# Kernel tuning notes

Hardware: AMD Instinct MI355X
Metric: run time of the kernel (lower is better)

Reference implementation:

```python
import jax, jax.numpy as jnp
import numpy as np

# dims: T time steps, B batch, CIN/COUT conv channels, HxW spatial, K kernel
T, B, CIN, COUT, H, Wd, K = 10, 32, 3, 64, 64, 64, 3
DECAY = 0.2      # LIF leak factor
INH = 1.625      # lateral inhibition strength (mode='threshold')


def setup_inputs() -> dict:
    key = jax.random.key(0)
    k1, k2 = jax.random.split(key)
    x = (jax.random.uniform(k1, (T, B, CIN, H, Wd)) < 0.2).astype(jnp.float32)
    W = jax.random.normal(k2, (COUT, CIN, K, K), dtype=jnp.float32)
    # normweight(): zero-mean, unit-std (biased) per output filter
    W = W - W.mean(axis=(1, 2, 3), keepdims=True)
    W = W / W.reshape(COUT, -1).std(axis=1).reshape(COUT, 1, 1, 1)
    return {"x": x, "W": W}


def _conv(x, W):
    # Conv2d stride=1, padding=1, no bias, NCHW/OIHW
    return jax.lax.conv_general_dilated(
        x, W, window_strides=(1, 1), padding=((1, 1), (1, 1)),
        dimension_numbers=("NCHW", "OIHW", "NCHW"))


def reference(x, W):
    def step(mem, x_t):
        i = _conv(x_t, W)                                        # (B,COUT,H,W)
        # ATB: adaptive per-channel threshold = max over batch+spatial
        thr = jnp.max(i, axis=(0, 2, 3), keepdims=True) + 1e-4   # (1,COUT,1,1)
        # ASF: clamp then thresholded sigmoid filter
        cur = jnp.maximum(i, 0.0)
        i_asf = thr * jax.nn.sigmoid((cur - 0.4 * thr) * (8.0 / thr))
        # LIF update with threshold = thr (set by ATB)
        mem = mem * DECAY + i_asf
        s = (mem > thr).astype(mem.dtype)                        # spikes 0/1
        # WTA k=1: keep only the strongest spiking channel per location
        score = mem * s
        winner = jnp.argmax(score, axis=1)                       # (B,H,W)
        oh = jnp.moveaxis(jax.nn.one_hot(winner, COUT, dtype=mem.dtype), -1, 1)
        s = s * oh
        # membrane reset of fired neurons
        mem = mem * (1.0 - s)
        # lateral inhibition: suppress non-winners at spiking locations
        any_sp = jnp.max(s, axis=1, keepdims=True)
        mem = mem - INH * thr * any_sp * (1.0 - s)
        return mem, s

    mem0 = jnp.zeros((B, COUT, H, Wd), jnp.float32)
    _, spikes = jax.lax.scan(step, mem0, x)
    return spikes  # (T,B,COUT,H,W)
```

## Files before the change

kernel.cpp:

```cpp
#include <hip/hip_runtime.h>
#include <math.h>

#define TT 10
#define BB 32
#define CIN 3
#define COUT 64
#define HH 64
#define WW 64
#define HW (HH*WW)
#define DECAY 0.2f
#define INH 1.625f

typedef __attribute__((ext_vector_type(2))) float f32x2;

__device__ __forceinline__ unsigned int enc_f(float f) {
    unsigned int u = __float_as_uint(f);
    return (u & 0x80000000u) ? ~u : (u | 0x80000000u);
}
__device__ __forceinline__ float dec_f(unsigned int u) {
    u = (u & 0x80000000u) ? (u & 0x7FFFFFFFu) : ~u;
    return __uint_as_float(u);
}

__device__ __forceinline__ void pkfma_lo(f32x2& acc, f32x2 w2, f32x2 x2) {
    asm("v_pk_fma_f32 %0, %1, %2, %0 op_sel:[0,0,0] op_sel_hi:[0,1,1]"
        : "+v"(acc) : "v"(w2), "v"(x2));
}
__device__ __forceinline__ void pkfma_hi(f32x2& acc, f32x2 w2, f32x2 x2) {
    asm("v_pk_fma_f32 %0, %1, %2, %0 op_sel:[1,0,0] op_sel_hi:[1,1,1]"
        : "+v"(acc) : "v"(w2), "v"(x2));
}
#define CONV_TAP(ACC, FI, X2) { if ((FI) & 1) pkfma_hi(ACC, wp[(FI)>>1], X2); \
                                else          pkfma_lo(ACC, wp[(FI)>>1], X2); }

#define CKH(RP, FB)                                                           \
    {                                                                         \
        const float* rpf_ = (const float*)(RP);                              \
        float4 q0_ = *(const float4*)(rpf_ + 0);                              \
        float4 q1_ = *(const float4*)(rpf_ + 4);                              \
        float4 q2_ = *(const float4*)(rpf_ + 8);                              \
        float4 q3_ = *(const float4*)(rpf_ + 12);                             \
        float4 q4_ = *(const float4*)(rpf_ + 16);                             \
        f32x2 d0 = {q0_.x, q0_.y}, d1 = {q0_.z, q0_.w},                       \
              d2 = {q1_.x, q1_.y}, d3 = {q1_.z, q1_.w},                       \
              d4 = {q2_.x, q2_.y}, d5 = {q2_.z, q2_.w},                       \
              d6 = {q3_.x, q3_.y}, d7 = {q3_.z, q3_.w},                       \
              d8 = {q4_.x, q4_.y}, d9 = {q4_.z, q4_.w};                       \
        CONV_TAP(a0, (FB)+0, d0); CONV_TAP(a0, (FB)+1, d1); CONV_TAP(a0, (FB)+2, d2); \
        CONV_TAP(a1, (FB)+0, d1); CONV_TAP(a1, (FB)+1, d2); CONV_TAP(a1, (FB)+2, d3); \
        CONV_TAP(a2, (FB)+0, d2); CONV_TAP(a2, (FB)+1, d3); CONV_TAP(a2, (FB)+2, d4); \
        CONV_TAP(a3, (FB)+0, d3); CONV_TAP(a3, (FB)+1, d4); CONV_TAP(a3, (FB)+2, d5); \
        CONV_TAP(a4, (FB)+0, d4); CONV_TAP(a4, (FB)+1, d5); CONV_TAP(a4, (FB)+2, d6); \
        CONV_TAP(a5, (FB)+0, d5); CONV_TAP(a5, (FB)+1, d6); CONV_TAP(a5, (FB)+2, d7); \
        CONV_TAP(a6, (FB)+0, d6); CONV_TAP(a6, (FB)+1, d7); CONV_TAP(a6, (FB)+2, d8); \
        CONV_TAP(a7, (FB)+0, d7); CONV_TAP(a7, (FB)+1, d8); CONV_TAP(a7, (FB)+2, d9); \
    }

#define LOAD_WP                                                               \
    f32x2 wp[14];                                                             \
    {                                                                         \
        const float* wl = Wt + lane * 27;                                     \
        _Pragma("unroll")                                                     \
        for (int k = 0; k < 13; k++) { f32x2 t_; t_.x = wl[2*k]; t_.y = wl[2*k+1]; wp[k] = t_; } \
        { f32x2 t_; t_.x = wl[26]; t_.y = wl[26]; wp[13] = t_; }              \
    }

__global__ __launch_bounds__(256) void thr_kernel(
    const float* __restrict__ x,
    const float* __restrict__ Wt,
    unsigned int* __restrict__ thr_raw,
    float* __restrict__ out)
{
    __shared__ f32x2 sx[CIN][6][68];
    __shared__ float wmax[4][2][COUT];

    const int tid  = threadIdx.x;
    const int lane = tid & 63;
    const int wave = tid >> 6;
    const int h0   = blockIdx.x * 4;
    const int b    = blockIdx.y;
    const int t0   = blockIdx.z * 2;

    LOAD_WP

    const float* xb0 = x + ((size_t)t0 * BB + b) * (CIN * HW);
    const float* xb1 = xb0 + (size_t)BB * CIN * HW;
    for (int l = tid; l < CIN * 6 * 66; l += 256) {
        int ci  = l / 396;
        int r   = (l % 396) / 66;
        int col = l % 66;
        int gh = h0 + r - 1;
        int gw = col - 1;
        f32x2 v; v.x = 0.f; v.y = 0.f;
        if (gh >= 0 && gh < HH && gw >= 0 && gw < WW) {
            size_t off = (size_t)ci * HW + gh * WW + gw;
            v.x = xb0[off];
            v.y = xb1[off];
        }
        sx[ci][r][col] = v;
    }
    __syncthreads();

    float mx0 = -INFINITY, mx1 = -INFINITY;

    for (int cc = 0; cc < 8; cc++) {
        #pragma unroll
        for (int k = 0; k < 4; k++) {
            int l   = cc * 1024 + k * 256 + tid;
            int th  = l >> 12;
            int row = (l >> 4) & 255;
            int q   = l & 15;
            int c   = row >> 2;
            int hr  = row & 3;
            float* ob = out + (((size_t)(t0 + th) * BB + b) * COUT) * HW;
            *(float4*)(ob + (size_t)c * HW + (h0 + hr) * WW + q * 4) =
                make_float4(0.f, 0.f, 0.f, 0.f);
        }

        f32x2 a0={0.f,0.f},a1={0.f,0.f},a2={0.f,0.f},a3={0.f,0.f},
              a4={0.f,0.f},a5={0.f,0.f},a6={0.f,0.f},a7={0.f,0.f};
        #pragma unroll
        for (int ci = 0; ci < CIN; ci++)
            #pragma unroll
            for (int kh = 0; kh < 3; kh++)
                CKH(&sx[ci][wave + kh][cc * 8], ci * 9 + kh * 3);

        mx0 = fmaxf(mx0, fmaxf(fmaxf(fmaxf(a0.x,a1.x),fmaxf(a2.x,a3.x)),
                               fmaxf(fmaxf(a4.x,a5.x),fmaxf(a6.x,a7.x))));
        mx1 = fmaxf(mx1, fmaxf(fmaxf(fmaxf(a0.y,a1.y),fmaxf(a2.y,a3.y)),
                               fmaxf(fmaxf(a4.y,a5.y),fmaxf(a6.y,a7.y))));
    }

    wmax[wave][0][lane] = mx0;
    wmax[wave][1][lane] = mx1;
    __syncthreads();
    if (wave < 2) {
        float m = fmaxf(fmaxf(wmax[0][wave][lane], wmax[1][wave][lane]),
                        fmaxf(wmax[2][wave][lane], wmax[3][wave][lane]));
        atomicMax(&thr_raw[(t0 + wave) * COUT + lane], enc_f(m));
    }
}

__global__ __launch_bounds__(256) void fused_kernel(
    const float* __restrict__ x,
    const float* __restrict__ Wt,
    const unsigned int* __restrict__ thr_raw,
    float* __restrict__ out)
{
    __shared__ f32x2 sx[5][CIN][3][36];

    const int tid  = threadIdx.x;
    const int lane = tid & 63;
    const int wave = tid >> 6;
    const int p0   = __builtin_amdgcn_readfirstlane(wave * 8);
    const int b    = blockIdx.x >> 7;
    const int h    = (blockIdx.x >> 1) & 63;
    const int w0   = (blockIdx.x & 1) << 5;

    LOAD_WP

    {
        const float* xb0 = x + (size_t)b * (CIN * HW);
        const size_t ts = (size_t)BB * CIN * HW;
        for (int l = tid; l < 5 * 306; l += 256) {
            int tp  = l / 306;
            int r0  = l - tp * 306;
            int ci  = r0 / 102;
            int r1  = r0 - ci * 102;
            int r   = r1 / 34;
            int col = r1 - r * 34;
            int gh = h + r - 1;
            int gw = w0 + col - 1;
            f32x2 v; v.x = 0.f; v.y = 0.f;
            if (gh >= 0 && gh < HH && gw >= 0 && gw < WW) {
                size_t off = (size_t)ci * HW + gh * WW + gw;
                v.x = xb0[(size_t)(2 * tp)     * ts + off];
                v.y = xb0[(size_t)(2 * tp + 1) * ts + off];
            }
            sx[tp][ci][r][col] = v;
        }
    }

    float mem[8];
    #pragma unroll
    for (int j = 0; j < 8; j++) mem[j] = 0.f;

    __syncthreads();

#define LIF_M(J, V) {                                                      \
        float cur = fmaxf(V, 0.f);                                         \
        float z   = (cur - s04) * sinv;                                    \
        float sig = 1.0f / (1.0f + expf(-z));                              \
        mv[J] = mem[J] * DECAY + thr * sig;                                \
        spor |= (mv[J] > thr) ? 1 : 0;                                     \
    }
#define LIF_W(J) {                                                         \
        float m   = mv[J];                                                 \
        int   sp  = m > thr;                                               \
        float score = sp ? m : 0.f;                                        \
        unsigned long long blt = __ballot(sp);                             \
        int fr = 0, sp_any = 0;                                            \
        if (blt) {                                                         \
            float bs = score;                                              \
            int   bc = lane;                                               \
            _Pragma("unroll")                                              \
            for (int off = 32; off > 0; off >>= 1) {                       \
                float so = __shfl_xor(bs, off, 64);                        \
                int   co = __shfl_xor(bc, off, 64);                        \
                if (so > bs || (so == bs && co < bc)) { bs = so; bc = co; }\
            }                                                              \
            int spw = __shfl(sp, bc, 64);     \
            fr     = (lane == bc) && sp;                                   \
            sp_any = spw;                                                  \
        }                                                                  \
        mem[J] = fr ? 0.f : (m - (sp_any ? sinh_ : 0.f));                  \
        if (fr) fmask |= (1 << (J));                                       \
    }

#define LIF_T(TIDX, F)                                                     \
    {                                                                      \
        float thr   = dec_f(F) + 1e-4f;                                    \
        float sinv  = 8.0f / thr;                                          \
        float s04   = 0.4f * thr;                                          \
        float sinh_ = INH * thr;                                           \
        int spor = 0;                                                      \
        float mv[8];                                                       \
        LIF_M(0, a0.SEL); LIF_M(1, a1.SEL); LIF_M(2, a2.SEL); LIF_M(3, a3.SEL); \
        LIF_M(4, a4.SEL); LIF_M(5, a5.SEL); LIF_M(6, a6.SEL); LIF_M(7, a7.SEL); \
        if (__ballot(spor)) {    \
            int fmask = 0;                                                 \
            LIF_W(0); LIF_W(1); LIF_W(2); LIF_W(3);                        \
            LIF_W(4); LIF_W(5); LIF_W(6); LIF_W(7);                        \
            if (fmask) {                                                   \
                float* os = out + (((size_t)(TIDX) * BB + b) * COUT) * HW  \
                          + h * WW + w0;                                   \
                _Pragma("unroll")                                          \
                for (int j = 0; j < 8; j++)                                \
                    if (fmask & (1 << j))                                  \
                        os[(size_t)lane * HW + p0 + j] = 1.0f;             \
            }                                                              \
        } else {                                                           \
            _Pragma("unroll")                                              \
            for (int j = 0; j < 8; j++) mem[j] = mv[j];                    \
        }                                                                  \
    }

    #pragma unroll 1
    for (int tp = 0; tp < 5; tp++) {
        unsigned int tru0 = thr_raw[(2 * tp)     * COUT + lane];
        unsigned int tru1 = thr_raw[(2 * tp + 1) * COUT + lane];

        f32x2 a0={0.f,0.f},a1={0.f,0.f},a2={0.f,0.f},a3={0.f,0.f},
              a4={0.f,0.f},a5={0.f,0.f},a6={0.f,0.f},a7={0.f,0.f};
        #pragma unroll
        for (int ci = 0; ci < CIN; ci++)
            #pragma unroll
            for (int kh = 0; kh < 3; kh++)
                CKH(&sx[tp][ci][kh][p0], ci * 9 + kh * 3);

#define SEL x
        LIF_T(2 * tp, tru0)
#undef SEL
#define SEL y
        LIF_T(2 * tp + 1, tru1)
#undef SEL
    }
#undef LIF_T
#undef LIF_W
#undef LIF_M
}

extern "C" void kernel_launch(void* const* d_in, const int* in_sizes, int n_in,
                              void* d_out, int out_size, void* d_ws, size_t ws_size,
                              hipStream_t stream) {
    const float* x = (const float*)d_in[0];
    const float* W = (const float*)d_in[1];
    float* out     = (float*)d_out;

    unsigned int* thr = (unsigned int*)d_ws;
    hipMemsetAsync(thr, 0, TT * COUT * sizeof(unsigned int), stream);

    thr_kernel<<<dim3(HH / 4, BB, TT / 2), 256, 0, stream>>>(x, W, thr, out);
    fused_kernel<<<dim3(BB * HH * 2), 256, 0, stream>>>(x, W, thr, out);
}
```

Baseline: 493.5 us.

## Remap threshold conv to lane-per-column with DPP wave max reduction

```diff
diff --git a/kernel.cpp b/kernel.cpp
--- a/kernel.cpp
+++ b/kernel.cpp
@@ -30,6 +30,17 @@
     asm("v_pk_fma_f32 %0, %1, %2, %0 op_sel:[1,0,0] op_sel_hi:[1,1,1]"
         : "+v"(acc) : "v"(w2), "v"(x2));
 }
+
+#define DPP_FMAX(V, CTRL) {                                                   \
+    int o_ = __builtin_amdgcn_update_dpp(__float_as_int(V), __float_as_int(V),\
+                                         (CTRL), 0xf, 0xf, false);            \
+    V = fmaxf(V, __int_as_float(o_)); }
+__device__ __forceinline__ float wave_fmax(float v) {
+    DPP_FMAX(v, 0x121); DPP_FMAX(v, 0x122); DPP_FMAX(v, 0x124);
+    DPP_FMAX(v, 0x128); DPP_FMAX(v, 0x142); DPP_FMAX(v, 0x143);
+    return v;
+}
+
 #define CONV_TAP(ACC, FI, X2) { if ((FI) & 1) pkfma_hi(ACC, wp[(FI)>>1], X2); \
                                 else          pkfma_lo(ACC, wp[(FI)>>1], X2); }
 
@@ -72,7 +83,7 @@
     float* __restrict__ out)
 {
     __shared__ f32x2 sx[CIN][6][68];
-    __shared__ float wmax[4][2][COUT];
+    __shared__ f32x2 wmaxL[4][COUT];
 
     const int tid  = threadIdx.x;
     const int lane = tid & 63;
@@ -80,8 +91,6 @@
     const int h0   = blockIdx.x * 4;
     const int b    = blockIdx.y;
     const int t0   = blockIdx.z * 2;
-
-    LOAD_WP
 
     const float* xb0 = x + ((size_t)t0 * BB + b) * (CIN * HW);
     const float* xb1 = xb0 + (size_t)BB * CIN * HW;
@@ -101,42 +110,63 @@
     }
     __syncthreads();
 
-    float mx0 = -INFINITY, mx1 = -INFINITY;
-
-    for (int cc = 0; cc < 8; cc++) {
+    f32x2 tp_[CIN][3][3];
+    #pragma unroll
+    for (int ci = 0; ci < CIN; ci++)
         #pragma unroll
-        for (int k = 0; k < 4; k++) {
-            int l   = cc * 1024 + k * 256 + tid;
+        for (int kh = 0; kh < 3; kh++)
+            #pragma unroll
+            for (int kw = 0; kw < 3; kw++)
+                tp_[ci][kh][kw] = sx[ci][wave + kh][lane + kw];
+
+    float* ob0 = out + (((size_t)t0 * BB + b) * COUT) * HW;
+    float* ob1 = ob0 + (size_t)BB * COUT * HW;
+
+    #pragma unroll 2
+    for (int c = 0; c < COUT; c++) {
+        if (c < 32) {
+            int l   = c * 256 + tid;
             int th  = l >> 12;
             int row = (l >> 4) & 255;
             int q   = l & 15;
-            int c   = row >> 2;
+            int cch = row >> 2;
             int hr  = row & 3;
-            float* ob = out + (((size_t)(t0 + th) * BB + b) * COUT) * HW;
-            *(float4*)(ob + (size_t)c * HW + (h0 + hr) * WW + q * 4) =
+            float* ob = th ? ob1 : ob0;
+            *(float4*)(ob + (size_t)cch * HW + (h0 + hr) * WW + q * 4) =
                 make_float4(0.f, 0.f, 0.f, 0.f);
         }
 
-        f32x2 a0={0.f,0.f},a1={0.f,0.f},a2={0.f,0.f},a3={0.f,0.f},
-              a4={0.f,0.f},a5={0.f,0.f},a6={0.f,0.f},a7={0.f,0.f};
+        const float* wl = Wt + c * 27;
+        float ax = 0.f, ay = 0.f;
         #pragma unroll
         for (int ci = 0; ci < CIN; ci++)
             #pragma unroll
             for (int kh = 0; kh < 3; kh++)
-                CKH(&sx[ci][wave + kh][cc * 8], ci * 9 + kh * 3);
-
-        mx0 = fmaxf(mx0, fmaxf(fmaxf(fmaxf(a0.x,a1.x),fmaxf(a2.x,a3.x)),
-                               fmaxf(fmaxf(a4.x,a5.x),fmaxf(a6.x,a7.x))));
-        mx1 = fmaxf(mx1, fmaxf(fmaxf(fmaxf(a0.y,a1.y),fmaxf(a2.y,a3.y)),
-                               fmaxf(fmaxf(a4.y,a5.y),fmaxf(a6.y,a7.y))));
-    }
-
-    wmax[wave][0][lane] = mx0;
-    wmax[wave][1][lane] = mx1;
+                #pragma unroll
+                for (int kw = 0; kw < 3; kw++) {
+                    float ws = wl[ci * 9 + kh * 3 + kw];
+                    f32x2 tv = tp_[ci][kh][kw];
+                    ax = fmaf(ws, tv.x, ax);
+                    ay = fmaf(ws, tv.y, ay);
+                }
+
+        float g0 = wave_fmax(ax);
+        float g1 = wave_fmax(ay);
+        int b0 = __builtin_amdgcn_readlane(__float_as_int(g0), 63);
+        int b1 = __builtin_amdgcn_readlane(__float_as_int(g1), 63);
+        if (lane == 0) {
+            f32x2 g; g.x = __int_as_float(b0); g.y = __int_as_float(b1);
+            wmaxL[wave][c] = g;
+        }
+    }
+
     __syncthreads();
     if (wave < 2) {
-        float m = fmaxf(fmaxf(wmax[0][wave][lane], wmax[1][wave][lane]),
-                        fmaxf(wmax[2][wave][lane], wmax[3][wave][lane]));
+        f32x2 m0 = wmaxL[0][lane], m1 = wmaxL[1][lane],
+              m2 = wmaxL[2][lane], m3 = wmaxL[3][lane];
+        float m = (wave == 0)
+                ? fmaxf(fmaxf(m0.x, m1.x), fmaxf(m2.x, m3.x))
+                : fmaxf(fmaxf(m0.y, m1.y), fmaxf(m2.y, m3.y));
         atomicMax(&thr_raw[(t0 + wave) * COUT + lane], enc_f(m));
     }
 }
@@ -216,7 +246,6 @@
         mem[J] = fr ? 0.f : (m - (sp_any ? sinh_ : 0.f));                  \
         if (fr) fmask |= (1 << (J));                                       \
     }
-
 #define LIF_T(TIDX, F)                                                     \
     {                                                                      \
         float thr   = dec_f(F) + 1e-4f;                                    \
```

Result: slower. 568.8 us (+15.3%).
